# Performance work log

Hardware: AMD Instinct MI355X
Metric: run time of the kernel (lower is better)

The kernel has to match this reference:

```python
import jax, jax.numpy as jnp
import numpy as np

D_MODEL = 512
HIDDEN_MULT = 4
D_FF = D_MODEL * HIDDEN_MULT
B, L = 4, 1024


def setup_inputs() -> dict:
    key = jax.random.key(0)
    ks = jax.random.split(key, 7)
    s1 = 1.0 / np.sqrt(D_MODEL)
    s2 = 1.0 / np.sqrt(D_FF)
    return {
        "x": jax.random.normal(ks[0], (B, L, D_MODEL), dtype=jnp.float32),
        "W1": jax.random.uniform(ks[1], (D_FF, D_MODEL), minval=-s1, maxval=s1, dtype=jnp.float32),
        "b1": jax.random.uniform(ks[2], (D_FF,), minval=-s1, maxval=s1, dtype=jnp.float32),
        "W2": jax.random.uniform(ks[3], (D_MODEL, D_FF), minval=-s2, maxval=s2, dtype=jnp.float32),
        "b2": jax.random.uniform(ks[4], (D_MODEL,), minval=-s2, maxval=s2, dtype=jnp.float32),
        "Lambda_raw_F": jax.random.uniform(ks[5], (D_FF, D_MODEL), minval=-3.0, maxval=3.0, dtype=jnp.float32),
        "Gamma_F": jax.random.uniform(ks[6], (D_FF, D_MODEL), minval=-0.5 * s1, maxval=0.5 * s1, dtype=jnp.float32),
    }


def _stp_forward(x, W1, b1, W2, b2, Lambda_raw_F, Gamma_F):
    # x: (B, L, D)
    retention = 1.0 - jax.nn.sigmoid(Lambda_raw_F)  # (d_ff, D)
    gamma = Gamma_F
    # static contribution of W1: (B, L, d_ff)
    static_h = jnp.einsum('bld,fd->blf', x, W1) + b1

    def step(F_state, inputs):
        # F_state: (B, d_ff, D); x_t: (B, D); sh_t: (B, d_ff)
        x_t, sh_t = inputs
        h_pre = sh_t + jnp.einsum('bfd,bd->bf', F_state, x_t)
        h = jax.nn.gelu(h_pre, approximate=False)
        out = jnp.einsum('bf,df->bd', h, W2) + b2
        # Hebbian outer-product update
        F_new = retention[None] * F_state + gamma[None] * (h_pre[:, :, None] * x_t[:, None, :])
        return F_new, out

    F0 = jnp.zeros((x.shape[0], W1.shape[0], W1.shape[1]), dtype=x.dtype)
    xs = (jnp.swapaxes(x, 0, 1), jnp.swapaxes(static_h, 0, 1))  # (L, B, ...)
    _, ys = jax.lax.scan(step, F0, xs)
    return jnp.swapaxes(ys, 0, 1)  # (B, L, D)


def reference(x, W1, b1, W2, b2, Lambda_raw_F, Gamma_F):
    return _stp_forward(x, W1, b1, W2, b2, Lambda_raw_F, Gamma_F)
```

## Files before the change

kernel.cpp:

```cpp
#include <hip/hip_runtime.h>
#include <cstdint>

#define DM   512
#define DFF  2048
#define BSZ  4
#define LSEQ 1024

typedef __attribute__((ext_vector_type(2))) float f32x2;

__device__ __forceinline__ f32x2 pk_mul(f32x2 a, f32x2 b) {
    f32x2 d;
    asm("v_pk_mul_f32 %0, %1, %2" : "=v"(d) : "v"(a), "v"(b));
    return d;
}
__device__ __forceinline__ f32x2 pk_fma(f32x2 a, f32x2 b, f32x2 c) {
    f32x2 d;
    asm("v_pk_fma_f32 %0, %1, %2, %3" : "=v"(d) : "v"(a), "v"(b), "v"(c));
    return d;
}
__device__ __forceinline__ f32x2 pk_add(f32x2 a, f32x2 b) {
    f32x2 d;
    asm("v_pk_add_f32 %0, %1, %2" : "=v"(d) : "v"(a), "v"(b));
    return d;
}

#define DPP_ADD(p, ctrl)                                                     \
    p += __int_as_float(__builtin_amdgcn_update_dpp(                         \
        0, __float_as_int(p), (ctrl), 0xF, 0xF, true))

__global__ __launch_bounds__(256, 4)
void stp_scan(const float* __restrict__ x,
              const float* __restrict__ Lam,
              const float* __restrict__ Gam,
              float* __restrict__ hbuf)
{
    const int tid  = threadIdx.x;
    const int lane = tid & 63;
    const int wid  = tid >> 6;
    const int j    = lane & 31;
    const int h    = lane >> 5;
    const int b    = blockIdx.x >> 8;
    const int f    = ((blockIdx.x & 255) << 3) + (wid << 1) + h;

    __shared__ float4 xs[2][128];

    const float4* __restrict__ x4g =
        reinterpret_cast<const float4*>(x + (size_t)b * LSEQ * DM);
    float* __restrict__ hbase = hbuf + (size_t)b * LSEQ * DFF;

    f32x2 F[8], R[8], G[8];
    {
        const float4* lr = reinterpret_cast<const float4*>(Lam + (size_t)f * DM);
        const float4* gr = reinterpret_cast<const float4*>(Gam + (size_t)f * DM);
        #pragma unroll
        for (int k = 0; k < 4; ++k) {
            float4 lv = lr[j + 32 * k];
            float4 gv = gr[j + 32 * k];
            f32x2 r0, r1;
            r0.x = 1.0f / (1.0f + expf(lv.x));
            r0.y = 1.0f / (1.0f + expf(lv.y));
            r1.x = 1.0f / (1.0f + expf(lv.z));
            r1.y = 1.0f / (1.0f + expf(lv.w));
            R[2 * k] = r0;   R[2 * k + 1] = r1;
            f32x2 g0; g0.x = gv.x; g0.y = gv.y;
            f32x2 g1; g1.x = gv.z; g1.y = gv.w;
            G[2 * k] = g0;   G[2 * k + 1] = g1;
            f32x2 z; z.x = 0.f; z.y = 0.f;
            F[2 * k] = z;    F[2 * k + 1] = z;
        }
    }

#define STP_STEP(T, CUR, SHV)                                                 \
    {                                                                         \
        float4 q0 = xs[CUR][j];                                               \
        float4 q1 = xs[CUR][j + 32];                                          \
        float4 q2 = xs[CUR][j + 64];                                          \
        float4 q3 = xs[CUR][j + 96];                                          \
        f32x2 x0 = *(f32x2*)&q0.x, x1 = *(f32x2*)&q0.z;                       \
        f32x2 x2 = *(f32x2*)&q1.x, x3 = *(f32x2*)&q1.z;                       \
        f32x2 x4_ = *(f32x2*)&q2.x, x5 = *(f32x2*)&q2.z;                      \
        f32x2 x6 = *(f32x2*)&q3.x, x7 = *(f32x2*)&q3.z;                       \
        f32x2 a0 = pk_mul(F[0], x0); f32x2 a1 = pk_mul(F[2], x2);             \
        a0 = pk_fma(F[1], x1, a0);   a1 = pk_fma(F[3], x3, a1);               \
        a0 = pk_fma(F[4], x4_, a0);  a1 = pk_fma(F[5], x5, a1);               \
        a0 = pk_fma(F[6], x6, a0);   a1 = pk_fma(F[7], x7, a1);               \
        f32x2 asum = pk_add(a0, a1);                                          \
        float p = asum.x + asum.y;                                            \
        DPP_ADD(p, 0x111);                                    \
        DPP_ADD(p, 0x112);                                    \
        DPP_ADD(p, 0x114);                                    \
        DPP_ADD(p, 0x118);                                    \
        DPP_ADD(p, 0x142);            \
        float hpv = __int_as_float(                                           \
            __builtin_amdgcn_ds_swizzle(__float_as_int(p), 0x3E0)) + (SHV);   \
        if (j == 0) hbase[(size_t)(T) * DFF + f] = hpv;                       \
        f32x2 hp2; hp2.x = hpv; hp2.y = hpv;                                  \
        F[0] = pk_fma(pk_mul(G[0], x0), hp2, pk_mul(R[0], F[0]));             \
        F[1] = pk_fma(pk_mul(G[1], x1), hp2, pk_mul(R[1], F[1]));             \
        F[2] = pk_fma(pk_mul(G[2], x2), hp2, pk_mul(R[2], F[2]));             \
        F[3] = pk_fma(pk_mul(G[3], x3), hp2, pk_mul(R[3], F[3]));             \
        F[4] = pk_fma(pk_mul(G[4], x4_), hp2, pk_mul(R[4], F[4]));            \
        F[5] = pk_fma(pk_mul(G[5], x5), hp2, pk_mul(R[5], F[5]));             \
        F[6] = pk_fma(pk_mul(G[6], x6), hp2, pk_mul(R[6], F[6]));             \
        F[7] = pk_fma(pk_mul(G[7], x7), hp2, pk_mul(R[7], F[7]));             \
    }

    float4 stgA, stgB;
    if (tid < 128) {
        xs[0][tid] = x4g[tid];
        stgA = x4g[128 + tid];
    }
    float shA = hbase[f];
    float shB = hbase[(size_t)DFF + f];
    __syncthreads();

    #pragma unroll 1
    for (int t = 0; t < LSEQ; t += 2) {
        STP_STEP(t, 0, shA)
        if (tid < 128) xs[1][tid] = stgA;
        __syncthreads();
        {
            const int tl = (t + 2 < LSEQ) ? t + 2 : LSEQ - 1;
            if (tid < 128) stgB = x4g[tl * 128 + tid];
            shA = hbase[(size_t)tl * DFF + f];
        }
        STP_STEP(t + 1, 1, shB)
        if (tid < 128) xs[0][tid] = stgB;
        __syncthreads();
        {
            const int tl = (t + 3 < LSEQ) ? t + 3 : LSEQ - 1;
            if (tid < 128) stgA = x4g[tl * 128 + tid];
            shB = hbase[(size_t)tl * DFF + f];
        }
    }
#undef STP_STEP
}

__global__ __launch_bounds__(256)
void gelu_inplace(float4* __restrict__ p, int n4)
{
    int i = blockIdx.x * blockDim.x + threadIdx.x;
    const int stride = gridDim.x * blockDim.x;
    for (; i < n4; i += stride) {
        float4 v = p[i];
        v.x = 0.5f * v.x * (1.0f + erff(v.x * 0.70710678118654752f));
        v.y = 0.5f * v.y * (1.0f + erff(v.y * 0.70710678118654752f));
        v.z = 0.5f * v.z * (1.0f + erff(v.z * 0.70710678118654752f));
        v.w = 0.5f * v.w * (1.0f + erff(v.w * 0.70710678118654752f));
        p[i] = v;
    }
}

__global__ __launch_bounds__(256)
void gemm_nt_bias(const float* __restrict__ A,
                  const float* __restrict__ Bm,
                  const float* __restrict__ bias,
                  float* __restrict__ C,
                  int M, int N, int K)
{
    __shared__ float As[16][68];
    __shared__ float Bs[16][68];

    const int tid = threadIdx.x;
    const int tx  = tid & 15;
    const int ty  = tid >> 4;
    const int row0 = blockIdx.y * 64;
    const int col0 = blockIdx.x * 64;

    const int lr = tid >> 2;
    const int lk = (tid & 3) << 2;

    const float* Aptr = A  + (size_t)(row0 + lr) * K + lk;
    const float* Bptr = Bm + (size_t)(col0 + lr) * K + lk;

    float acc[4][4] = {};
    float4 av = *reinterpret_cast<const float4*>(Aptr);
    float4 bv = *reinterpret_cast<const float4*>(Bptr);

    const int NT = K >> 4;
    for (int kt = 0; kt < NT; ++kt) {
        __syncthreads();
        As[lk + 0][lr] = av.x; As[lk + 1][lr] = av.y;
        As[lk + 2][lr] = av.z; As[lk + 3][lr] = av.w;
        Bs[lk + 0][lr] = bv.x; Bs[lk + 1][lr] = bv.y;
        Bs[lk + 2][lr] = bv.z; Bs[lk + 3][lr] = bv.w;
        __syncthreads();

        if (kt + 1 < NT) {
            av = *reinterpret_cast<const float4*>(Aptr + (kt + 1) * 16);
            bv = *reinterpret_cast<const float4*>(Bptr + (kt + 1) * 16);
        }

        #pragma unroll
        for (int k = 0; k < 16; ++k) {
            float4 a = *reinterpret_cast<const float4*>(&As[k][ty * 4]);
            float4 bb = *reinterpret_cast<const float4*>(&Bs[k][tx * 4]);
            acc[0][0] = fmaf(a.x, bb.x, acc[0][0]);
            acc[0][1] = fmaf(a.x, bb.y, acc[0][1]);
            acc[0][2] = fmaf(a.x, bb.z, acc[0][2]);
            acc[0][3] = fmaf(a.x, bb.w, acc[0][3]);
            acc[1][0] = fmaf(a.y, bb.x, acc[1][0]);
            acc[1][1] = fmaf(a.y, bb.y, acc[1][1]);
            acc[1][2] = fmaf(a.y, bb.z, acc[1][2]);
            acc[1][3] = fmaf(a.y, bb.w, acc[1][3]);
            acc[2][0] = fmaf(a.z, bb.x, acc[2][0]);
            acc[2][1] = fmaf(a.z, bb.y, acc[2][1]);
            acc[2][2] = fmaf(a.z, bb.z, acc[2][2]);
            acc[2][3] = fmaf(a.z, bb.w, acc[2][3]);
            acc[3][0] = fmaf(a.w, bb.x, acc[3][0]);
            acc[3][1] = fmaf(a.w, bb.y, acc[3][1]);
            acc[3][2] = fmaf(a.w, bb.z, acc[3][2]);
            acc[3][3] = fmaf(a.w, bb.w, acc[3][3]);
        }
    }

    const float4 bb = *reinterpret_cast<const float4*>(&bias[col0 + tx * 4]);
    #pragma unroll
    for (int i = 0; i < 4; ++i) {
        float4 o;
        o.x = acc[i][0] + bb.x;
        o.y = acc[i][1] + bb.y;
        o.z = acc[i][2] + bb.z;
        o.w = acc[i][3] + bb.w;
        *reinterpret_cast<float4*>(&C[(size_t)(row0 + ty * 4 + i) * N + col0 + tx * 4]) = o;
    }
}

extern "C" void kernel_launch(void* const* d_in, const int* in_sizes, int n_in,
                              void* d_out, int out_size, void* d_ws, size_t ws_size,
                              hipStream_t stream)
{
    const float* x   = (const float*)d_in[0];
    const float* W1  = (const float*)d_in[1];
    const float* b1  = (const float*)d_in[2];
    const float* W2  = (const float*)d_in[3];
    const float* b2  = (const float*)d_in[4];
    const float* Lam = (const float*)d_in[5];
    const float* Gam = (const float*)d_in[6];
    float* out  = (float*)d_out;
    float* hbuf = (float*)d_ws;

    const int M = BSZ * LSEQ;

    gemm_nt_bias<<<dim3(DFF / 64, M / 64), dim3(256), 0, stream>>>(
        x, W1, b1, hbuf, M, DFF, DM);

    stp_scan<<<dim3(BSZ * (DFF / 8)), dim3(256), 0, stream>>>(x, Lam, Gam, hbuf);

    gelu_inplace<<<dim3(2048), dim3(256), 0, stream>>>(
        reinterpret_cast<float4*>(hbuf), M * DFF / 4);

    gemm_nt_bias<<<dim3(DM / 64, M / 64), dim3(256), 0, stream>>>(
        hbuf, W2, b2, out, M, DM, DFF);
}
```

Measured before the change: 777.9 us.

## Stage x in 8-step chunks to cut per-step barriers in scan kernel

The recurrent scan now stages eight timesteps of x into LDS per double-buffered chunk, instead of one step at a time. Block-wide barriers drop from one per step to one per chunk, and the static-h values for the next chunk are prefetched into registers. The cost is a larger LDS footprint (32KB per block), which may limit occupancy, plus extra registers for the prefetched values.

```diff
diff --git a/kernel.cpp b/kernel.cpp
--- a/kernel.cpp
+++ b/kernel.cpp
@@ -5,6 +5,8 @@
 #define DFF  2048
 #define BSZ  4
 #define LSEQ 1024
+#define CHUNK 8
+#define NCHUNK (LSEQ / CHUNK)
 
 typedef __attribute__((ext_vector_type(2))) float f32x2;
 
@@ -42,7 +44,7 @@
     const int b    = blockIdx.x >> 8;
     const int f    = ((blockIdx.x & 255) << 3) + (wid << 1) + h;
 
-    __shared__ float4 xs[2][128];
+    __shared__ float4 xs[2][CHUNK * 128];
 
     const float4* __restrict__ x4g =
         reinterpret_cast<const float4*>(x + (size_t)b * LSEQ * DM);
@@ -70,70 +72,84 @@
         }
     }
 
-#define STP_STEP(T, CUR, SHV)                                                 \
-    {                                                                         \
-        float4 q0 = xs[CUR][j];                                               \
-        float4 q1 = xs[CUR][j + 32];                                          \
-        float4 q2 = xs[CUR][j + 64];                                          \
-        float4 q3 = xs[CUR][j + 96];                                          \
-        f32x2 x0 = *(f32x2*)&q0.x, x1 = *(f32x2*)&q0.z;                       \
-        f32x2 x2 = *(f32x2*)&q1.x, x3 = *(f32x2*)&q1.z;                       \
-        f32x2 x4_ = *(f32x2*)&q2.x, x5 = *(f32x2*)&q2.z;                      \
-        f32x2 x6 = *(f32x2*)&q3.x, x7 = *(f32x2*)&q3.z;                       \
-        f32x2 a0 = pk_mul(F[0], x0); f32x2 a1 = pk_mul(F[2], x2);             \
-        a0 = pk_fma(F[1], x1, a0);   a1 = pk_fma(F[3], x3, a1);               \
-        a0 = pk_fma(F[4], x4_, a0);  a1 = pk_fma(F[5], x5, a1);               \
-        a0 = pk_fma(F[6], x6, a0);   a1 = pk_fma(F[7], x7, a1);               \
-        f32x2 asum = pk_add(a0, a1);                                          \
-        float p = asum.x + asum.y;                                            \
-        DPP_ADD(p, 0x111);                                    \
-        DPP_ADD(p, 0x112);                                    \
-        DPP_ADD(p, 0x114);                                    \
-        DPP_ADD(p, 0x118);                                    \
-        DPP_ADD(p, 0x142);            \
-        float hpv = __int_as_float(                                           \
-            __builtin_amdgcn_ds_swizzle(__float_as_int(p), 0x3E0)) + (SHV);   \
-        if (j == 0) hbase[(size_t)(T) * DFF + f] = hpv;                       \
-        f32x2 hp2; hp2.x = hpv; hp2.y = hpv;                                  \
-        F[0] = pk_fma(pk_mul(G[0], x0), hp2, pk_mul(R[0], F[0]));             \
-        F[1] = pk_fma(pk_mul(G[1], x1), hp2, pk_mul(R[1], F[1]));             \
-        F[2] = pk_fma(pk_mul(G[2], x2), hp2, pk_mul(R[2], F[2]));             \
-        F[3] = pk_fma(pk_mul(G[3], x3), hp2, pk_mul(R[3], F[3]));             \
-        F[4] = pk_fma(pk_mul(G[4], x4_), hp2, pk_mul(R[4], F[4]));            \
-        F[5] = pk_fma(pk_mul(G[5], x5), hp2, pk_mul(R[5], F[5]));             \
-        F[6] = pk_fma(pk_mul(G[6], x6), hp2, pk_mul(R[6], F[6]));             \
-        F[7] = pk_fma(pk_mul(G[7], x7), hp2, pk_mul(R[7], F[7]));             \
-    }
-
-    float4 stgA, stgB;
-    if (tid < 128) {
-        xs[0][tid] = x4g[tid];
-        stgA = x4g[128 + tid];
-    }
-    float shA = hbase[f];
-    float shB = hbase[(size_t)DFF + f];
+    float4 s0, s1, s2, s3;
+    {
+        const float4* xsp = x4g + tid;
+        float4 t0 = xsp[0], t1 = xsp[256], t2 = xsp[512], t3 = xsp[768];
+        float4* xw = &xs[0][0];
+        xw[tid] = t0; xw[tid + 256] = t1; xw[tid + 512] = t2; xw[tid + 768] = t3;
+        s0 = xsp[1024]; s1 = xsp[1280]; s2 = xsp[1536]; s3 = xsp[1792];
+    }
+    float shc[CHUNK], shn[CHUNK];
+    #pragma unroll
+    for (int k = 0; k < CHUNK; ++k) shc[k] = hbase[(size_t)k * DFF + f];
     __syncthreads();
 
+    float* pst = hbase + f;
+
     #pragma unroll 1
-    for (int t = 0; t < LSEQ; t += 2) {
-        STP_STEP(t, 0, shA)
-        if (tid < 128) xs[1][tid] = stgA;
+    for (int c = 0; c < NCHUNK; ++c) {
+        const float4* __restrict__ xb = &xs[c & 1][0];
+        const int cn = (c + 1 < NCHUNK) ? (c + 1) : 0;
+        const float* pp = hbase + f + (size_t)cn * (CHUNK * DFF);
+
+        #pragma unroll
+        for (int s = 0; s < CHUNK; ++s) {
+            float4 q0 = xb[s * 128 + j];
+            float4 q1 = xb[s * 128 + j + 32];
+            float4 q2 = xb[s * 128 + j + 64];
+            float4 q3 = xb[s * 128 + j + 96];
+            shn[s] = *pp; pp += DFF;
+
+            f32x2 x0 = *(f32x2*)&q0.x, x1 = *(f32x2*)&q0.z;
+            f32x2 x2 = *(f32x2*)&q1.x, x3 = *(f32x2*)&q1.z;
+            f32x2 x4_ = *(f32x2*)&q2.x, x5 = *(f32x2*)&q2.z;
+            f32x2 x6 = *(f32x2*)&q3.x, x7 = *(f32x2*)&q3.z;
+
+            f32x2 a0 = pk_mul(F[0], x0); f32x2 a1 = pk_mul(F[2], x2);
+            a0 = pk_fma(F[1], x1, a0);   a1 = pk_fma(F[3], x3, a1);
+            a0 = pk_fma(F[4], x4_, a0);  a1 = pk_fma(F[5], x5, a1);
+            a0 = pk_fma(F[6], x6, a0);   a1 = pk_fma(F[7], x7, a1);
+            f32x2 asum = pk_add(a0, a1);
+            float p = asum.x + asum.y;
+
+            DPP_ADD(p, 0x111);
+            DPP_ADD(p, 0x112);
+            DPP_ADD(p, 0x114);
+            DPP_ADD(p, 0x118);
+            DPP_ADD(p, 0x142);
+            const float hpv = __int_as_float(
+                __builtin_amdgcn_ds_swizzle(__float_as_int(p), 0x3E0)) + shc[s];
+
+            if (j == 0) *pst = hpv;
+            pst += DFF;
+
+            f32x2 hp2; hp2.x = hpv; hp2.y = hpv;
+            F[0] = pk_fma(pk_mul(G[0], x0), hp2, pk_mul(R[0], F[0]));
+            F[1] = pk_fma(pk_mul(G[1], x1), hp2, pk_mul(R[1], F[1]));
+            F[2] = pk_fma(pk_mul(G[2], x2), hp2, pk_mul(R[2], F[2]));
+            F[3] = pk_fma(pk_mul(G[3], x3), hp2, pk_mul(R[3], F[3]));
+            F[4] = pk_fma(pk_mul(G[4], x4_), hp2, pk_mul(R[4], F[4]));
+            F[5] = pk_fma(pk_mul(G[5], x5), hp2, pk_mul(R[5], F[5]));
+            F[6] = pk_fma(pk_mul(G[6], x6), hp2, pk_mul(R[6], F[6]));
+            F[7] = pk_fma(pk_mul(G[7], x7), hp2, pk_mul(R[7], F[7]));
+        }
+
+        {
+            float4* xw = &xs[(c + 1) & 1][0];
+            xw[tid] = s0; xw[tid + 256] = s1;
+            xw[tid + 512] = s2; xw[tid + 768] = s3;
+        }
         __syncthreads();
+
         {
-            const int tl = (t + 2 < LSEQ) ? t + 2 : LSEQ - 1;
-            if (tid < 128) stgB = x4g[tl * 128 + tid];
-            shA = hbase[(size_t)tl * DFF + f];
-        }
-        STP_STEP(t + 1, 1, shB)
-        if (tid < 128) xs[0][tid] = stgB;
-        __syncthreads();
-        {
-            const int tl = (t + 3 < LSEQ) ? t + 3 : LSEQ - 1;
-            if (tid < 128) stgA = x4g[tl * 128 + tid];
-            shB = hbase[(size_t)tl * DFF + f];
-        }
-    }
-#undef STP_STEP
+            const int cp = (c + 2 < NCHUNK) ? (c + 2) : (NCHUNK - 1);
+            const float4* xsp = x4g + (size_t)cp * (CHUNK * 128) + tid;
+            s0 = xsp[0]; s1 = xsp[256]; s2 = xsp[512]; s3 = xsp[768];
+        }
+        #pragma unroll
+        for (int k = 0; k < CHUNK; ++k) shc[k] = shn[k];
+    }
 }
 
 __global__ __launch_bounds__(256)
```

Result: no change. 768.2 us (-1.2%).
